# Optimization experiments

Hardware: AMD Instinct MI355X
Metric: run time of the kernel (lower is better)

Reference implementation:

```python
import jax, jax.numpy as jnp
import numpy as np

STRIDE = 1
PADDING = 1
KERNEL = 3


def _extract_patches(x, k, stride, padding):
    # x: [N, C, H, W] -> patches stacked as [k, k, N, C, Hout, Wout]
    xp = jnp.pad(x, ((0, 0), (0, 0), (padding, padding), (padding, padding)))
    Hp, Wp = xp.shape[2], xp.shape[3]
    oh = (Hp - k) // stride + 1
    ow = (Wp - k) // stride + 1
    rows = []
    for i in range(k):
        cols = []
        for j in range(k):
            cols.append(xp[:, :, i : i + oh * stride : stride, j : j + ow * stride : stride])
        rows.append(jnp.stack(cols, axis=0))
    return jnp.stack(rows, axis=0)  # [k, k, N, C, oh, ow]


def setup_inputs() -> dict:
    key = jax.random.key(0)
    k1, k2 = jax.random.split(key)
    N, C, H, W = 32, 32, 56, 56
    O, OH, OW, K = 32, 56, 56, 3
    x = jax.random.normal(k1, (N, C, H, W), dtype=jnp.float32)
    # kaiming-normal-ish scale for leaky_relu(a=0.1), fan_out mode
    fan_out = O * K * K
    gain = np.sqrt(2.0 / (1.0 + 0.1 ** 2))
    std = gain / np.sqrt(fan_out)
    weight = jax.random.normal(k2, (O, OH, OW, C, K, K), dtype=jnp.float32) * std
    bias = jnp.zeros((1, O, OH, OW), dtype=jnp.float32)
    return {"x": x, "weight": weight, "bias": bias}


def reference(x, weight, bias):
    # weight: [O, H, W, C, i, k]; patches: [i, k, N, C, H, W]
    patches = _extract_patches(x, KERNEL, STRIDE, PADDING)
    out = jnp.einsum('ohwcik,iknchw->nohw', weight, patches)
    return out + bias
```

## Files before the change

kernel.cpp:

```cpp
#include <hip/hip_runtime.h>

#define N_  32
#define C_  32
#define H_  56
#define W_  56
#define O_  32
#define HP_ 58
#define WP_ 58
#define HW_ (H_*W_)
#define CHW_ (C_*H_*W_)
#define KK_ 9
#define CKK_ (C_*KK_)

#define XT_ELEMS ((size_t)C_*HP_*WP_*N_)

typedef __bf16 bf16x8 __attribute__((ext_vector_type(8)));
typedef float  f32x4  __attribute__((ext_vector_type(4)));

__global__ __launch_bounds__(256) void xpose_kernel(const float* __restrict__ x,
                                                    __bf16* __restrict__ xT) {
    const int c = blockIdx.x;
    const int y = blockIdx.y;
    __shared__ float sbuf[32 * 57];
    const int tid = threadIdx.x;
    const bool interior = (y >= 1) && (y <= H_);
    if (interior) {
        for (int idx = tid; idx < N_ * W_; idx += 256) {
            int n = idx / W_;
            int col = idx - n * W_;
            sbuf[n * 57 + col] = x[((size_t)(n * C_ + c) * H_ + (y - 1)) * W_ + col];
        }
    }
    __syncthreads();
    __bf16* dst = xT + ((size_t)(c * HP_ + y)) * WP_ * N_;
    for (int idx = tid; idx < WP_ * N_; idx += 256) {
        int xx = idx >> 5;
        int n  = idx & 31;
        float v = 0.f;
        if (interior && xx >= 1 && xx <= W_) v = sbuf[n * 57 + (xx - 1)];
        dst[idx] = (__bf16)v;
    }
}

__global__ __launch_bounds__(256) void lc2d_mfma(const float* __restrict__ wgt,
                                                 const __bf16* __restrict__ xT,
                                                 const float* __restrict__ bias,
                                                 float* __restrict__ out) {
    __shared__ int offs[288];
    __shared__ __align__(16) float sbuf[32][33][2];

    const int tid = threadIdx.x;
    for (int k = tid; k < 288; k += 256) {
        int c = k / 9, ij = k - 9 * c;
        int i = ij / 3, j = ij - 3 * i;
        offs[k] = c * (HP_ * WP_ * N_) + i * (WP_ * N_) + j * N_;
    }
    __syncthreads();

    const int flat = blockIdx.x;
    const int wg = (flat & 7) * 196 + (flat >> 3);
    const int wt = wg % 28;
    const int h  = wg / 28;
    const int wave = tid >> 6;
    const int lane = tid & 63;
    const int dw = wave & 1;
    const int oh = wave >> 1;
    const int w  = wt * 2 + dw;
    const int q = lane >> 4;
    const int r = lane & 15;

    const float* wb = wgt + ((size_t)((oh * 16 + r) * HW_ + h * W_ + w)) * CKK_ + 8 * q;
    const __bf16* ab = xT + (h * WP_ + w) * N_ + r;

    f32x4 acc0 = {0.f, 0.f, 0.f, 0.f};
    f32x4 acc1 = {0.f, 0.f, 0.f, 0.f};

    #pragma unroll
    for (int s = 0; s < 9; ++s) {
        const int4 ov0 = *(const int4*)&offs[32 * s + 8 * q];
        const int4 ov1 = *(const int4*)&offs[32 * s + 8 * q + 4];
        const float4 ba = *(const float4*)(wb + 32 * s);
        const float4 bb = *(const float4*)(wb + 32 * s + 4);

        const int offv[8] = {ov0.x, ov0.y, ov0.z, ov0.w, ov1.x, ov1.y, ov1.z, ov1.w};
        bf16x8 af0, af1, bfB;
        #pragma unroll
        for (int t = 0; t < 8; ++t) {
            const __bf16* p = ab + offv[t];
            af0[t] = p[0];
            af1[t] = p[16];
        }
        bfB[0] = (__bf16)ba.x; bfB[1] = (__bf16)ba.y; bfB[2] = (__bf16)ba.z; bfB[3] = (__bf16)ba.w;
        bfB[4] = (__bf16)bb.x; bfB[5] = (__bf16)bb.y; bfB[6] = (__bf16)bb.z; bfB[7] = (__bf16)bb.w;

        acc0 = __builtin_amdgcn_mfma_f32_16x16x32_bf16(af0, bfB, acc0, 0, 0, 0);
        acc1 = __builtin_amdgcn_mfma_f32_16x16x32_bf16(af1, bfB, acc1, 0, 0, 0);
    }

    #pragma unroll
    for (int mt = 0; mt < 2; ++mt) {
        f32x4 a = mt == 0 ? acc0 : acc1;
        const int o = oh * 16 + r;
        #pragma unroll
        for (int reg = 0; reg < 4; ++reg) {
            const int n = mt * 16 + q * 4 + reg;
            sbuf[n][o][dw] = a[reg];
        }
    }
    __syncthreads();

    const int w0 = wt * 2;
    #pragma unroll
    for (int rr = 0; rr < 4; ++rr) {
        const int fl = rr * 256 + tid;
        const int n = fl >> 5;
        const int o = fl & 31;
        float2 v = *(const float2*)&sbuf[n][o][0];
        const float2 bv = *(const float2*)(bias + o * HW_ + h * W_ + w0);
        v.x += bv.x; v.y += bv.y;
        *(float2*)(out + (size_t)n * CHW_ + o * HW_ + h * W_ + w0) = v;
    }
}

__global__ __launch_bounds__(256) void lc2d_naive(const float* __restrict__ x,
                                                  const float* __restrict__ wgt,
                                                  const float* __restrict__ bias,
                                                  float* __restrict__ out) {
    int idx = blockIdx.x * 256 + threadIdx.x;
    const int total = N_ * O_ * H_ * W_;
    if (idx >= total) return;
    int w = idx % W_;
    int h = (idx / W_) % H_;
    int o = (idx / HW_) % O_;
    int n = idx / CHW_;
    const float* wp = wgt + ((size_t)((o * H_ + h) * W_ + w)) * CKK_;
    float s = 0.f;
    for (int c = 0; c < C_; ++c) {
        for (int i = 0; i < 3; ++i) {
            int yy = h + i - 1;
            if (yy < 0 || yy >= H_) continue;
            for (int j = 0; j < 3; ++j) {
                int xx = w + j - 1;
                if (xx < 0 || xx >= W_) continue;
                s = fmaf(wp[c * KK_ + i * 3 + j],
                         x[((size_t)(n * C_ + c) * H_ + yy) * W_ + xx], s);
            }
        }
    }
    out[idx] = s + bias[idx % CHW_];
}

extern "C" void kernel_launch(void* const* d_in, const int* in_sizes, int n_in,
                              void* d_out, int out_size, void* d_ws, size_t ws_size,
                              hipStream_t stream) {
    const float* x    = (const float*)d_in[0];
    const float* wgt  = (const float*)d_in[1];
    const float* bias = (const float*)d_in[2];
    float* out = (float*)d_out;

    const size_t need = XT_ELEMS * sizeof(__bf16);
    if (ws_size >= need) {
        __bf16* xT = (__bf16*)d_ws;
        hipLaunchKernelGGL(xpose_kernel, dim3(C_, HP_), dim3(256), 0, stream, x, xT);
        hipLaunchKernelGGL(lc2d_mfma, dim3(1568), dim3(256), 0, stream, wgt, xT, bias, out);
    } else {
        int total = N_ * O_ * H_ * W_;
        hipLaunchKernelGGL(lc2d_naive, dim3((total + 255) / 256), dim3(256), 0, stream,
                           x, wgt, bias, out);
    }
}
```

Baseline: 42.09 us.

## Stage A operand in LDS with vectorized loads and bf16 pair packing

Before the MFMA loop, each block now cooperatively loads the needed input patch rows from the transposed bf16 buffer with 16-byte loads. It packs pairs of k-values into 32-bit words and stores them in a padded shared-memory buffer. The MFMA loop then reads A fragments as four 32-bit LDS loads instead of sixteen scattered 2-byte global loads. This adds a shared-memory staging phase, an extra barrier and about 41KB of LDS, which may reduce occupancy.

```diff
diff --git a/kernel.cpp b/kernel.cpp
--- a/kernel.cpp
+++ b/kernel.cpp
@@ -13,6 +13,9 @@
 #define CKK_ (C_*KK_)
 
 #define XT_ELEMS ((size_t)C_*HP_*WP_*N_)
+
+#define KP_   144
+#define PSTR_ 36
 
 typedef __bf16 bf16x8 __attribute__((ext_vector_type(8)));
 typedef float  f32x4  __attribute__((ext_vector_type(4)));
@@ -47,6 +50,7 @@
                                                  const float* __restrict__ bias,
                                                  float* __restrict__ out) {
     __shared__ int offs[288];
+    __shared__ unsigned P2[2 * KP_ * PSTR_];
     __shared__ __align__(16) float sbuf[32][33][2];
 
     const int tid = threadIdx.x;
@@ -61,40 +65,59 @@
     const int wg = (flat & 7) * 196 + (flat >> 3);
     const int wt = wg % 28;
     const int h  = wg / 28;
+    const int w0 = wt * 2;
+
+    const __bf16* xbase = xT + (h * WP_ + w0) * N_;
+    for (int task = tid; task < 1152; task += 256) {
+        const int dw  = task / 576;
+        const int rem = task - dw * 576;
+        const int kp  = rem >> 2;
+        const int g   = rem & 3;
+        const __bf16* s0 = xbase + dw * N_ + offs[2 * kp]     + 8 * g;
+        const __bf16* s1 = xbase + dw * N_ + offs[2 * kp + 1] + 8 * g;
+        union { uint4 q; ushort s[8]; } ua, ub;
+        ua.q = *(const uint4*)s0;
+        ub.q = *(const uint4*)s1;
+        unsigned o0[8];
+        #pragma unroll
+        for (int m = 0; m < 8; ++m)
+            o0[m] = (unsigned)ua.s[m] | ((unsigned)ub.s[m] << 16);
+        unsigned* dst = &P2[(dw * KP_ + kp) * PSTR_ + 8 * g];
+        *(uint4*)(dst)     = make_uint4(o0[0], o0[1], o0[2], o0[3]);
+        *(uint4*)(dst + 4) = make_uint4(o0[4], o0[5], o0[6], o0[7]);
+    }
+    __syncthreads();
+
     const int wave = tid >> 6;
     const int lane = tid & 63;
     const int dw = wave & 1;
     const int oh = wave >> 1;
-    const int w  = wt * 2 + dw;
+    const int w  = w0 + dw;
     const int q = lane >> 4;
     const int r = lane & 15;
 
     const float* wb = wgt + ((size_t)((oh * 16 + r) * HW_ + h * W_ + w)) * CKK_ + 8 * q;
-    const __bf16* ab = xT + (h * WP_ + w) * N_ + r;
+    const unsigned* pa = &P2[(dw * KP_ + 4 * q) * PSTR_ + r];
 
     f32x4 acc0 = {0.f, 0.f, 0.f, 0.f};
     f32x4 acc1 = {0.f, 0.f, 0.f, 0.f};
 
     #pragma unroll
     for (int s = 0; s < 9; ++s) {
-        const int4 ov0 = *(const int4*)&offs[32 * s + 8 * q];
-        const int4 ov1 = *(const int4*)&offs[32 * s + 8 * q + 4];
+        union { unsigned u[4]; bf16x8 v; } a0, a1;
+        #pragma unroll
+        for (int d = 0; d < 4; ++d) {
+            a0.u[d] = pa[s * (16 * PSTR_) + d * PSTR_];
+            a1.u[d] = pa[s * (16 * PSTR_) + d * PSTR_ + 16];
+        }
         const float4 ba = *(const float4*)(wb + 32 * s);
         const float4 bb = *(const float4*)(wb + 32 * s + 4);
-
-        const int offv[8] = {ov0.x, ov0.y, ov0.z, ov0.w, ov1.x, ov1.y, ov1.z, ov1.w};
-        bf16x8 af0, af1, bfB;
-        #pragma unroll
-        for (int t = 0; t < 8; ++t) {
-            const __bf16* p = ab + offv[t];
-            af0[t] = p[0];
-            af1[t] = p[16];
-        }
+        bf16x8 bfB;
         bfB[0] = (__bf16)ba.x; bfB[1] = (__bf16)ba.y; bfB[2] = (__bf16)ba.z; bfB[3] = (__bf16)ba.w;
         bfB[4] = (__bf16)bb.x; bfB[5] = (__bf16)bb.y; bfB[6] = (__bf16)bb.z; bfB[7] = (__bf16)bb.w;
 
-        acc0 = __builtin_amdgcn_mfma_f32_16x16x32_bf16(af0, bfB, acc0, 0, 0, 0);
-        acc1 = __builtin_amdgcn_mfma_f32_16x16x32_bf16(af1, bfB, acc1, 0, 0, 0);
+        acc0 = __builtin_amdgcn_mfma_f32_16x16x32_bf16(a0.v, bfB, acc0, 0, 0, 0);
+        acc1 = __builtin_amdgcn_mfma_f32_16x16x32_bf16(a1.v, bfB, acc1, 0, 0, 0);
     }
 
     #pragma unroll
@@ -109,7 +132,6 @@
     }
     __syncthreads();
 
-    const int w0 = wt * 2;
     #pragma unroll
     for (int rr = 0; rr < 4; ++rr) {
         const int fl = rr * 256 + tid;
```

New measurement: 41.70 us. About the same (-0.9%).
